# Kernel tuning notes

Measured on AMD Instinct MI355X. Metric: run time of the kernel, lower is better.

Reference implementation:

```python
import jax, jax.numpy as jnp
import numpy as np
from jax import lax

B, C, H, W = 32, 684, 16, 64
HID, A, CK, K = 256, 512, 512, 11


def setup_inputs() -> dict:
    key = jax.random.key(0)
    ks = jax.random.split(key, 12)
    s = 0.02
    return {
        "cnn_features": jax.random.normal(ks[0], (B, C, H, W), jnp.float32),
        "hidden": jax.random.normal(ks[1], (B, HID), jnp.float32),
        "alpha_sum": jax.random.uniform(ks[2], (B, 1, H, W), jnp.float32),
        "image_mask": jnp.ones((B, 1, H, W), jnp.float32),
        # hidden_weight: Linear(HID -> A)
        "Wh": jax.random.normal(ks[3], (A, HID), jnp.float32) * s,
        "bh": jnp.zeros((A,), jnp.float32),
        # encoder_feature_conv: Conv2d(C -> A, 1x1) == pointwise linear
        "Wec": jax.random.normal(ks[4], (A, C), jnp.float32) * s,
        "bec": jnp.zeros((A,), jnp.float32),
        # attention_conv: Conv2d(1 -> CK, 11x11, pad 5, no bias)
        "Wac": jax.random.normal(ks[5], (CK, 1, K, K), jnp.float32) * s,
        # attention_weight: Linear(CK -> A, no bias)
        "Waw": jax.random.normal(ks[6], (A, CK), jnp.float32) * s,
        # alpha_convert: Linear(A -> 1)
        "Wv": jax.random.normal(ks[7], (1, A), jnp.float32) * s,
        "bv": jnp.zeros((1,), jnp.float32),
    }


def reference(cnn_features, hidden, alpha_sum, image_mask,
              Wh, bh, Wec, bec, Wac, Waw, Wv, bv):
    # query = hidden_weight(hidden): [B, A]
    query = hidden @ Wh.T + bh
    # attention_conv(alpha_sum): [B, CK, H, W]
    ast = lax.conv_general_dilated(
        alpha_sum, Wac, window_strides=(1, 1),
        padding=[(K // 2, K // 2), (K // 2, K // 2)],
        dimension_numbers=("NCHW", "OIHW", "NCHW"))
    # attention_weight on permuted conv output: [B, H, W, A]
    coverage_alpha = jnp.einsum("bkhw,ak->bhwa", ast, Waw)
    # encoder_feature_conv (1x1 conv == pointwise linear): [B, H, W, A]
    cnn_trans = jnp.einsum("bchw,ac->bhwa", cnn_features, Wec) + bec
    # additive attention score
    alpha_score = jnp.tanh(query[:, None, None, :] + coverage_alpha + cnn_trans)
    # alpha_convert -> scalar energy per position: [B, H, W]
    energy = jnp.einsum("bhwa,a->bhw", alpha_score, Wv[0]) + bv[0]
    energy = energy - energy.max()  # global max-subtract as in original
    energy_exp = jnp.exp(energy) * image_mask[:, 0]
    denom = energy_exp.sum(axis=(-1, -2))[:, None, None] + 1e-10
    alpha = energy_exp / denom  # [B, H, W]
    alpha_sum_new = alpha[:, None, :, :] + alpha_sum  # [B, 1, H, W]
    # context: weighted spatial sum over features -> [B, C]
    context_vector = jnp.einsum("bhw,bchw->bc", alpha, cnn_features)
    return (context_vector, alpha, alpha_sum_new)
```

## Files before the change

kernel.cpp:

```cpp
#include <hip/hip_runtime.h>
#include <math.h>

#define Bn   32
#define Cn   684
#define Hn   16
#define Wn   64
#define HWn  1024
#define HIDn 256
#define An   512
#define KKn  121
#define CREAL 805
#define CPAD 832
#define NSTEP 26
#define NBLK 256

#define OUT_ALPHA 21888
#define OUT_ASUM  (21888 + 32768)

typedef short short8 __attribute__((ext_vector_type(8)));
typedef float floatx4 __attribute__((ext_vector_type(4)));

__device__ __forceinline__ unsigned short f2bf(float f) {
    union { float f; unsigned int i; } v; v.f = f;
    unsigned int i = v.i;
    return (unsigned short)((i + 0x7fffu + ((i >> 16) & 1u)) >> 16);
}
__device__ __forceinline__ unsigned int pack2bf(float v0, float v1) {
    unsigned int u0 = __float_as_uint(v0), u1 = __float_as_uint(v1);
    u0 = (u0 + 0x7fffu + ((u0 >> 16) & 1u)) >> 16;
    u1 = (u1 + 0x7fffu + ((u1 >> 16) & 1u)) & 0xffff0000u;
    return u0 | u1;
}
__device__ __forceinline__ void async_lds16(void* lds, const void* g) {
    __builtin_amdgcn_global_load_lds(
        (const __attribute__((address_space(1))) unsigned int*)g,
        (__attribute__((address_space(3))) unsigned int*)lds, 16, 0, 0);
}

__global__ __launch_bounds__(256) void k_prep(
    const float* __restrict__ hidden,
    const float* __restrict__ Wh,
    const float* __restrict__ bh,
    const float* __restrict__ bec,
    const float* __restrict__ Wec,
    const float* __restrict__ Wac,
    const float* __restrict__ Waw,
    float* __restrict__ query,
    unsigned short* __restrict__ VTbf)
{
    __shared__ float sbuf[512];
    const int blk = blockIdx.x, t = threadIdx.x;
    if (blk < 512) {
        const int a = blk;
        sbuf[t]       = Waw[(size_t)a * 512 + t];
        sbuf[t + 256] = Waw[(size_t)a * 512 + t + 256];
        __syncthreads();
        for (int cp = t; cp < Cn; cp += 256)
            VTbf[(size_t)a * CPAD + cp] = f2bf(Wec[(size_t)a * Cn + cp]);
        if (t < KKn) {
            float s = 0.f;
            #pragma unroll 8
            for (int k = 0; k < 512; ++k)
                s = fmaf(sbuf[k], Wac[k * KKn + t], s);
            VTbf[(size_t)a * CPAD + Cn + t] = f2bf(s);
        }
        for (int cp = CREAL + t; cp < CPAD; cp += 256)
            VTbf[(size_t)a * CPAD + cp] = 0;
    } else {
        const int b = blk - 512;
        sbuf[t] = (t < HIDn) ? hidden[b * HIDn + t] : 0.f;
        __syncthreads();
        for (int a = t; a < An; a += 256) {
            const float4* wp = (const float4*)(Wh + (size_t)a * HIDn);
            float s = bh[a] + bec[a];
            #pragma unroll 8
            for (int i = 0; i < HIDn / 4; ++i) {
                float4 w = wp[i];
                s = fmaf(sbuf[4 * i],     w.x, s);
                s = fmaf(sbuf[4 * i + 1], w.y, s);
                s = fmaf(sbuf[4 * i + 2], w.z, s);
                s = fmaf(sbuf[4 * i + 3], w.w, s);
            }
            query[b * An + a] = s;
        }
    }
}

__device__ __forceinline__ float fetchU(const float* __restrict__ X,
                                        const float* plane,
                                        int m, int row) {
    if (row < Cn)   return X[(size_t)row * HWn + m];
    if (row < CREAL) {
        int ij = row - Cn; int di = ij / 11, dj = ij - di * 11;
        return plane[di * 74 + m + dj];
    }
    return 0.f;
}

__global__ __launch_bounds__(256, 3) void k_energy(
    const float* __restrict__ X,
    const float* __restrict__ asum,
    const float* __restrict__ Wv,
    const float* __restrict__ query,
    const unsigned short* __restrict__ VTbf,
    float* __restrict__ energy)
{
    __shared__ unsigned short As[2 * 64 * 40];
    __shared__ unsigned short Bs[2 * 256 * 32];
    __shared__ float plane[11 * 74 + 2];
    __shared__ float qs[NBLK];
    __shared__ float wvs[NBLK];

    const int t = threadIdx.x;
    const int nh = blockIdx.x, hh = blockIdx.y, b = blockIdx.z;
    const int w = t >> 6, lane = t & 63;
    const int q = lane >> 4, r = lane & 15;
    const int nbase = nh * NBLK;
    const int mA = t & 63;
    const int koA = t >> 6;

    const float* Xb = X + (size_t)b * Cn * HWn + hh * Wn;

    for (int i = t; i < 11 * 74; i += 256) {
        int di = i / 74, cc = i - di * 74;
        int h2 = hh + di - 5, w2 = cc - 5;
        float v = 0.f;
        if (h2 >= 0 && h2 < Hn && w2 >= 0 && w2 < Wn)
            v = asum[b * HWn + h2 * Wn + w2];
        plane[i] = v;
    }
    qs[t]  = query[b * An + nbase + t];
    wvs[t] = Wv[nbase + t];
    {
        const float* xp = Xb + (size_t)(koA * 8) * HWn + mA;
        unsigned int pk[4];
        #pragma unroll
        for (int jj = 0; jj < 4; ++jj)
            pk[jj] = pack2bf(xp[(size_t)(2 * jj) * HWn], xp[(size_t)(2 * jj + 1) * HWn]);
        *(uint4*)&As[mA * 40 + koA * 8] = make_uint4(pk[0], pk[1], pk[2], pk[3]);
    }
    #pragma unroll
    for (int ii = 0; ii < 4; ++ii) {
        int n0 = w * 64 + ii * 16;
        int row = nbase + n0 + (lane >> 2);
        int gc = (lane & 3) ^ ((lane >> 2) & 3);
        async_lds16(&Bs[n0 * 32], VTbf + (size_t)row * CPAD + gc * 8);
    }
    __syncthreads();

    floatx4 acc[4][4];
    #pragma unroll
    for (int mf = 0; mf < 4; ++mf)
        #pragma unroll
        for (int nf = 0; nf < 4; ++nf)
            acc[mf][nf] = (floatx4){0.f, 0.f, 0.f, 0.f};

    for (int ch = 0; ch < NSTEP; ++ch) {
        const int cur = ch & 1;
        const unsigned short* Ab = As + cur * (64 * 40);
        const unsigned short* Bb = Bs + cur * (256 * 32);

        short8 af[4], bfr[4];
        #pragma unroll
        for (int mf = 0; mf < 4; ++mf)
            af[mf] = *(const short8*)&Ab[(mf * 16 + r) * 40 + q * 8];
        #pragma unroll
        for (int nf = 0; nf < 4; ++nf)
            bfr[nf] = *(const short8*)&Bb[(w * 64 + nf * 16 + r) * 32 + (q ^ (r & 3)) * 8];

        if (ch < NSTEP - 1) {
            const int c1 = (ch + 1) * 32;
            unsigned short* Bn_ = Bs + (cur ^ 1) * (256 * 32);
            #pragma unroll
            for (int ii = 0; ii < 4; ++ii) {
                int n0 = w * 64 + ii * 16;
                int row = nbase + n0 + (lane >> 2);
                int gc = (lane & 3) ^ ((lane >> 2) & 3);
                async_lds16(&Bn_[n0 * 32], VTbf + (size_t)row * CPAD + c1 + gc * 8);
            }
            unsigned int pk[4];
            if (c1 + 31 < Cn) {
                const float* xp = Xb + (size_t)(c1 + koA * 8) * HWn + mA;
                #pragma unroll
                for (int jj = 0; jj < 4; ++jj)
                    pk[jj] = pack2bf(xp[(size_t)(2 * jj) * HWn],
                                     xp[(size_t)(2 * jj + 1) * HWn]);
            } else {
                float v[8];
                #pragma unroll
                for (int jj = 0; jj < 8; ++jj)
                    v[jj] = fetchU(Xb, plane, mA, c1 + koA * 8 + jj);
                #pragma unroll
                for (int jj = 0; jj < 4; ++jj)
                    pk[jj] = pack2bf(v[2 * jj], v[2 * jj + 1]);
            }
            *(uint4*)&As[(cur ^ 1) * (64 * 40) + mA * 40 + koA * 8] =
                make_uint4(pk[0], pk[1], pk[2], pk[3]);
        }

        #pragma unroll
        for (int mf = 0; mf < 4; ++mf)
            #pragma unroll
            for (int nf = 0; nf < 4; ++nf)
                acc[mf][nf] = __builtin_amdgcn_mfma_f32_16x16x32_bf16(
                    af[mf], bfr[nf], acc[mf][nf], 0, 0, 0);

        __syncthreads();
    }

    float ep[16];
    #pragma unroll
    for (int i = 0; i < 16; ++i) ep[i] = 0.f;
    #pragma unroll
    for (int nf = 0; nf < 4; ++nf) {
        int nl = w * 64 + nf * 16 + r;
        float qv = qs[nl], wv = wvs[nl];
        #pragma unroll
        for (int mf = 0; mf < 4; ++mf)
            #pragma unroll
            for (int rg = 0; rg < 4; ++rg) {
                float x = acc[mf][nf][rg] + qv;
                float e2 = __expf(2.f * x);
                float th = 1.f - 2.f * __builtin_amdgcn_rcpf(e2 + 1.f);
                ep[mf * 4 + rg] += wv * th;
            }
    }
    float* red = (float*)Bs;
    #pragma unroll
    for (int mf = 0; mf < 4; ++mf)
        #pragma unroll
        for (int rg = 0; rg < 4; ++rg)
            red[(mf * 16 + q * 4 + rg) * 65 + w * 16 + r] = ep[mf * 4 + rg];
    __syncthreads();
    if (t < 64) {
        float s = 0.f;
        #pragma unroll 16
        for (int i = 0; i < 64; ++i) s += red[t * 65 + i];
        atomicAdd(&energy[b * HWn + hh * Wn + t], s);
    }
}

__global__ __launch_bounds__(256) void k_ctx(
    const float* __restrict__ X,
    const float* __restrict__ energy,
    const float* __restrict__ mask,
    const float* __restrict__ asum,
    float* __restrict__ out)
{
    __shared__ float al[1024];
    __shared__ float rsm[8];
    const int bx = blockIdx.x, b = blockIdx.y;
    const int t = threadIdx.x, lane = t & 63, wid = t >> 6;

    float e[4], ex[4];
    #pragma unroll
    for (int i = 0; i < 4; ++i) e[i] = energy[b * HWn + i * 256 + t];
    float m = fmaxf(fmaxf(e[0], e[1]), fmaxf(e[2], e[3]));
    for (int off = 32; off >= 1; off >>= 1) m = fmaxf(m, __shfl_down(m, off, 64));
    if (lane == 0) rsm[wid] = m;
    __syncthreads();
    if (t == 0)
        rsm[4] = fmaxf(fmaxf(rsm[0], rsm[1]), fmaxf(rsm[2], rsm[3]));
    __syncthreads();
    const float M = rsm[4];
    float s = 0.f;
    #pragma unroll
    for (int i = 0; i < 4; ++i) {
        ex[i] = expf(e[i] - M) * mask[b * HWn + i * 256 + t];
        s += ex[i];
    }
    for (int off = 32; off >= 1; off >>= 1) s += __shfl_down(s, off, 64);
    __syncthreads();
    if (lane == 0) rsm[wid] = s;
    __syncthreads();
    if (t == 0) rsm[5] = rsm[0] + rsm[1] + rsm[2] + rsm[3] + 1e-10f;
    __syncthreads();
    const float denom = rsm[5];
    #pragma unroll
    for (int i = 0; i < 4; ++i) al[i * 256 + t] = ex[i] / denom;
    __syncthreads();

    const int c = bx * 4 + wid;
    const float* xp = X + ((size_t)(b * Cn + c)) * HWn;
    float s2 = 0.f;
    #pragma unroll
    for (int i = 0; i < 4; ++i) {
        int off = i * 256 + lane * 4;
        float4 x = *(const float4*)(xp + off);
        float4 a = *(const float4*)(al + off);
        s2 = fmaf(a.x, x.x, s2);
        s2 = fmaf(a.y, x.y, s2);
        s2 = fmaf(a.z, x.z, s2);
        s2 = fmaf(a.w, x.w, s2);
    }
    for (int off = 32; off >= 1; off >>= 1) s2 += __shfl_down(s2, off, 64);
    if (lane == 0) out[b * Cn + c] = s2;

    if (bx == 0) {
        #pragma unroll
        for (int i = 0; i < 4; ++i) {
            int p = i * 256 + t;
            float a = al[p];
            out[OUT_ALPHA + b * HWn + p] = a;
            out[OUT_ASUM  + b * HWn + p] = a + asum[b * HWn + p];
        }
    }
}

extern "C" void kernel_launch(void* const* d_in, const int* in_sizes, int n_in,
                              void* d_out, int out_size, void* d_ws, size_t ws_size,
                              hipStream_t stream)
{
    const float* X      = (const float*)d_in[0];
    const float* hidden = (const float*)d_in[1];
    const float* asum   = (const float*)d_in[2];
    const float* mask   = (const float*)d_in[3];
    const float* Wh     = (const float*)d_in[4];
    const float* bh     = (const float*)d_in[5];
    const float* Wec    = (const float*)d_in[6];
    const float* bec    = (const float*)d_in[7];
    const float* Wac    = (const float*)d_in[8];
    const float* Waw    = (const float*)d_in[9];
    const float* Wv     = (const float*)d_in[10];
    (void)in_sizes; (void)n_in; (void)out_size; (void)ws_size;

    float* out = (float*)d_out;
    float* ws = (float*)d_ws;
    float* query  = ws;
    float* energy = ws + 16384;
    unsigned short* VTbf = (unsigned short*)(ws + 16384 + 32768);

    hipMemsetAsync(energy, 0, HWn * Bn * sizeof(float), stream);
    k_prep   <<<dim3(544),      dim3(256), 0, stream>>>(hidden, Wh, bh, bec,
                                                        Wec, Wac, Waw, query, VTbf);
    k_energy <<<dim3(2, 16, 32), dim3(256), 0, stream>>>(X, asum, Wv, query, VTbf, energy);
    k_ctx    <<<dim3(171, 32),  dim3(256), 0, stream>>>(X, energy, mask, asum, out);
}
```

Measured before the change: 252.9 us.

## Load B fragments directly to registers, prefetch X two steps ahead, drop atomics

The energy GEMM no longer stages the bf16 weight matrix through LDS with async loads. Each wave now loads its B fragments straight from global memory into registers, and the fp32 X loads are prefetched two K-steps ahead, which frees LDS and raises the occupancy hint to 4. The two N-halves write separate partial energy buffers that k_ctx sums, replacing atomicAdd and the memset. k_prep also tiles Wac through shared memory for the Waw·Wac fold. In exchange, B reads are uncoalesced, strided global loads per wave with no LDS reuse across waves, and register pressure rises.

```diff
diff --git a/kernel.cpp b/kernel.cpp
--- a/kernel.cpp
+++ b/kernel.cpp
@@ -31,11 +31,6 @@
     u1 = (u1 + 0x7fffu + ((u1 >> 16) & 1u)) & 0xffff0000u;
     return u0 | u1;
 }
-__device__ __forceinline__ void async_lds16(void* lds, const void* g) {
-    __builtin_amdgcn_global_load_lds(
-        (const __attribute__((address_space(1))) unsigned int*)g,
-        (__attribute__((address_space(3))) unsigned int*)lds, 16, 0, 0);
-}
 
 __global__ __launch_bounds__(256) void k_prep(
     const float* __restrict__ hidden,
@@ -49,21 +44,28 @@
     unsigned short* __restrict__ VTbf)
 {
     __shared__ float sbuf[512];
+    __shared__ float wac_s[64 * KKn];
     const int blk = blockIdx.x, t = threadIdx.x;
     if (blk < 512) {
         const int a = blk;
         sbuf[t]       = Waw[(size_t)a * 512 + t];
         sbuf[t + 256] = Waw[(size_t)a * 512 + t + 256];
-        __syncthreads();
         for (int cp = t; cp < Cn; cp += 256)
             VTbf[(size_t)a * CPAD + cp] = f2bf(Wec[(size_t)a * Cn + cp]);
-        if (t < KKn) {
-            float s = 0.f;
-            #pragma unroll 8
-            for (int k = 0; k < 512; ++k)
-                s = fmaf(sbuf[k], Wac[k * KKn + t], s);
+        float s = 0.f;
+        for (int kb = 0; kb < 8; ++kb) {
+            __syncthreads();
+            for (int i = t; i < 64 * KKn; i += 256)
+                wac_s[i] = Wac[kb * 64 * KKn + i];
+            __syncthreads();
+            if (t < KKn) {
+                #pragma unroll 8
+                for (int kk = 0; kk < 64; ++kk)
+                    s = fmaf(sbuf[kb * 64 + kk], wac_s[kk * KKn + t], s);
+            }
+        }
+        if (t < KKn)
             VTbf[(size_t)a * CPAD + Cn + t] = f2bf(s);
-        }
         for (int cp = CREAL + t; cp < CPAD; cp += 256)
             VTbf[(size_t)a * CPAD + cp] = 0;
     } else {
@@ -86,10 +88,10 @@
     }
 }
 
-__device__ __forceinline__ float fetchU(const float* __restrict__ X,
+__device__ __forceinline__ float fetchU(const float* __restrict__ Xb,
                                         const float* plane,
                                         int m, int row) {
-    if (row < Cn)   return X[(size_t)row * HWn + m];
+    if (row < Cn)   return Xb[(size_t)row * HWn + m];
     if (row < CREAL) {
         int ij = row - Cn; int di = ij / 11, dj = ij - di * 11;
         return plane[di * 74 + m + dj];
@@ -97,7 +99,7 @@
     return 0.f;
 }
 
-__global__ __launch_bounds__(256, 3) void k_energy(
+__global__ __launch_bounds__(256, 4) void k_energy(
     const float* __restrict__ X,
     const float* __restrict__ asum,
     const float* __restrict__ Wv,
@@ -106,7 +108,7 @@
     float* __restrict__ energy)
 {
     __shared__ unsigned short As[2 * 64 * 40];
-    __shared__ unsigned short Bs[2 * 256 * 32];
+    __shared__ float red[64 * 65];
     __shared__ float plane[11 * 74 + 2];
     __shared__ float qs[NBLK];
     __shared__ float wvs[NBLK];
@@ -120,6 +122,7 @@
     const int koA = t >> 6;
 
     const float* Xb = X + (size_t)b * Cn * HWn + hh * Wn;
+    const unsigned short* Bw = VTbf + (size_t)(nbase + w * 64) * CPAD;
 
     for (int i = t; i < 11 * 74; i += 256) {
         int di = i / 74, cc = i - di * 74;
@@ -131,6 +134,7 @@
     }
     qs[t]  = query[b * An + nbase + t];
     wvs[t] = Wv[nbase + t];
+
     {
         const float* xp = Xb + (size_t)(koA * 8) * HWn + mA;
         unsigned int pk[4];
@@ -139,13 +143,16 @@
             pk[jj] = pack2bf(xp[(size_t)(2 * jj) * HWn], xp[(size_t)(2 * jj + 1) * HWn]);
         *(uint4*)&As[mA * 40 + koA * 8] = make_uint4(pk[0], pk[1], pk[2], pk[3]);
     }
-    #pragma unroll
-    for (int ii = 0; ii < 4; ++ii) {
-        int n0 = w * 64 + ii * 16;
-        int row = nbase + n0 + (lane >> 2);
-        int gc = (lane & 3) ^ ((lane >> 2) & 3);
-        async_lds16(&Bs[n0 * 32], VTbf + (size_t)row * CPAD + gc * 8);
-    }
+    float xpref[8];
+    {
+        const float* xp = Xb + (size_t)(32 + koA * 8) * HWn + mA;
+        #pragma unroll
+        for (int jj = 0; jj < 8; ++jj) xpref[jj] = xp[(size_t)jj * HWn];
+    }
+    short8 bfr[4];
+    #pragma unroll
+    for (int nf = 0; nf < 4; ++nf)
+        bfr[nf] = *(const short8*)(Bw + (size_t)(nf * 16 + r) * CPAD + q * 8);
     __syncthreads();
 
     floatx4 acc[4][4];
@@ -157,54 +164,40 @@
 
     for (int ch = 0; ch < NSTEP; ++ch) {
         const int cur = ch & 1;
-        const unsigned short* Ab = As + cur * (64 * 40);
-        const unsigned short* Bb = Bs + cur * (256 * 32);
-
-        short8 af[4], bfr[4];
+        short8 af[4];
         #pragma unroll
         for (int mf = 0; mf < 4; ++mf)
-            af[mf] = *(const short8*)&Ab[(mf * 16 + r) * 40 + q * 8];
-        #pragma unroll
-        for (int nf = 0; nf < 4; ++nf)
-            bfr[nf] = *(const short8*)&Bb[(w * 64 + nf * 16 + r) * 32 + (q ^ (r & 3)) * 8];
-
-        if (ch < NSTEP - 1) {
-            const int c1 = (ch + 1) * 32;
-            unsigned short* Bn_ = Bs + (cur ^ 1) * (256 * 32);
-            #pragma unroll
-            for (int ii = 0; ii < 4; ++ii) {
-                int n0 = w * 64 + ii * 16;
-                int row = nbase + n0 + (lane >> 2);
-                int gc = (lane & 3) ^ ((lane >> 2) & 3);
-                async_lds16(&Bn_[n0 * 32], VTbf + (size_t)row * CPAD + c1 + gc * 8);
-            }
-            unsigned int pk[4];
-            if (c1 + 31 < Cn) {
-                const float* xp = Xb + (size_t)(c1 + koA * 8) * HWn + mA;
-                #pragma unroll
-                for (int jj = 0; jj < 4; ++jj)
-                    pk[jj] = pack2bf(xp[(size_t)(2 * jj) * HWn],
-                                     xp[(size_t)(2 * jj + 1) * HWn]);
-            } else {
-                float v[8];
-                #pragma unroll
-                for (int jj = 0; jj < 8; ++jj)
-                    v[jj] = fetchU(Xb, plane, mA, c1 + koA * 8 + jj);
-                #pragma unroll
-                for (int jj = 0; jj < 4; ++jj)
-                    pk[jj] = pack2bf(v[2 * jj], v[2 * jj + 1]);
-            }
-            *(uint4*)&As[(cur ^ 1) * (64 * 40) + mA * 40 + koA * 8] =
-                make_uint4(pk[0], pk[1], pk[2], pk[3]);
-        }
-
+            af[mf] = *(const short8*)&As[cur * (64 * 40) + (mf * 16 + r) * 40 + q * 8];
         #pragma unroll
         for (int mf = 0; mf < 4; ++mf)
             #pragma unroll
             for (int nf = 0; nf < 4; ++nf)
                 acc[mf][nf] = __builtin_amdgcn_mfma_f32_16x16x32_bf16(
                     af[mf], bfr[nf], acc[mf][nf], 0, 0, 0);
-
+        if (ch + 1 < NSTEP) {
+            const int c1 = (ch + 1) * 32;
+            #pragma unroll
+            for (int nf = 0; nf < 4; ++nf)
+                bfr[nf] = *(const short8*)(Bw + (size_t)(nf * 16 + r) * CPAD + c1 + q * 8);
+            unsigned int pk[4];
+            #pragma unroll
+            for (int jj = 0; jj < 4; ++jj)
+                pk[jj] = pack2bf(xpref[2 * jj], xpref[2 * jj + 1]);
+            *(uint4*)&As[(cur ^ 1) * (64 * 40) + mA * 40 + koA * 8] =
+                make_uint4(pk[0], pk[1], pk[2], pk[3]);
+        }
+        if (ch + 2 < NSTEP) {
+            const int c2 = (ch + 2) * 32;
+            if (c2 + 31 < Cn) {
+                const float* xp = Xb + (size_t)(c2 + koA * 8) * HWn + mA;
+                #pragma unroll
+                for (int jj = 0; jj < 8; ++jj) xpref[jj] = xp[(size_t)jj * HWn];
+            } else {
+                #pragma unroll
+                for (int jj = 0; jj < 8; ++jj)
+                    xpref[jj] = fetchU(Xb, plane, mA, c2 + koA * 8 + jj);
+            }
+        }
         __syncthreads();
     }
 
@@ -225,7 +218,6 @@
                 ep[mf * 4 + rg] += wv * th;
             }
     }
-    float* red = (float*)Bs;
     #pragma unroll
     for (int mf = 0; mf < 4; ++mf)
         #pragma unroll
@@ -236,7 +228,7 @@
         float s = 0.f;
         #pragma unroll 16
         for (int i = 0; i < 64; ++i) s += red[t * 65 + i];
-        atomicAdd(&energy[b * HWn + hh * Wn + t], s);
+        energy[(size_t)nh * (Bn * HWn) + b * HWn + hh * Wn + t] = s;
     }
 }
 
@@ -254,7 +246,10 @@
 
     float e[4], ex[4];
     #pragma unroll
-    for (int i = 0; i < 4; ++i) e[i] = energy[b * HWn + i * 256 + t];
+    for (int i = 0; i < 4; ++i) {
+        int p = b * HWn + i * 256 + t;
+        e[i] = energy[p] + energy[Bn * HWn + p];
+    }
     float m = fmaxf(fmaxf(e[0], e[1]), fmaxf(e[2], e[3]));
     for (int off = 32; off >= 1; off >>= 1) m = fmaxf(m, __shfl_down(m, off, 64));
     if (lane == 0) rsm[wid] = m;
@@ -328,11 +323,10 @@
     float* ws = (float*)d_ws;
     float* query  = ws;
     float* energy = ws + 16384;
-    unsigned short* VTbf = (unsigned short*)(ws + 16384 + 32768);
-
-    hipMemsetAsync(energy, 0, HWn * Bn * sizeof(float), stream);
-    k_prep   <<<dim3(544),      dim3(256), 0, stream>>>(hidden, Wh, bh, bec,
-                                                        Wec, Wac, Waw, query, VTbf);
+    unsigned short* VTbf = (unsigned short*)(ws + 16384 + 65536);
+
+    k_prep   <<<dim3(544),       dim3(256), 0, stream>>>(hidden, Wh, bh, bec,
+                                                         Wec, Wac, Waw, query, VTbf);
     k_energy <<<dim3(2, 16, 32), dim3(256), 0, stream>>>(X, asum, Wv, query, VTbf, energy);
-    k_ctx    <<<dim3(171, 32),  dim3(256), 0, stream>>>(X, energy, mask, asum, out);
-}
+    k_ctx    <<<dim3(171, 32),   dim3(256), 0, stream>>>(X, energy, mask, asum, out);
+}
```

After: 259.6 us. 2.6% more time.
